# Kernel optimization log

Hardware: AMD Instinct MI355X
Metric: run time of the kernel (lower is better)

Reference implementation:

```python
import jax, jax.numpy as jnp
import numpy as np

N_NODES = 50000
N_EDGES = 800000
D = 128
BATCHSIZE = 64


def setup_inputs() -> dict:
    key = jax.random.key(0)
    k1, k2, k3, k4 = jax.random.split(key, 4)
    x = jax.random.normal(k1, (N_NODES, D), dtype=jnp.float32)
    eps = jnp.zeros((1,), dtype=jnp.float32)
    W_pred = jax.random.normal(k2, (D, D), dtype=jnp.float32) * (1.0 / np.sqrt(D))
    b_pred = jnp.zeros((D,), dtype=jnp.float32)
    edge_index = jax.random.randint(k3, (2, N_EDGES), 0, N_NODES, dtype=jnp.int64)
    batch = jnp.sort(jax.random.randint(k4, (N_NODES,), 0, BATCHSIZE, dtype=jnp.int64))
    return {"x": x, "eps": eps, "W_pred": W_pred, "b_pred": b_pred,
            "edge_index": edge_index, "batch": batch}


def reference(x, eps, W_pred, b_pred, edge_index, batch):
    src, dst = edge_index[0], edge_index[1]
    # spmm: sum of neighbor features for each destination node [N, D]
    agg = jax.ops.segment_sum(x[src], dst, num_segments=N_NODES)
    # eps-weighted self update (apply_func=None, norm=None)
    out = (1.0 + eps) * x + agg
    out = jax.nn.relu(out)  # activation='relu'
    # linear_prediction then per-graph scatter-add pooling
    pooled = out @ W_pred + b_pred  # [N, pooled_features]
    pooled2 = jax.ops.segment_sum(pooled, batch, num_segments=BATCHSIZE)  # [B, pooled]
    return out, pooled2
```

## Files before the change

kernel.cpp:

```cpp
#include <hip/hip_runtime.h>
#include <hip/hip_bf16.h>

#define N_NODES 50000
#define N_EDGES 800000
#define D 128
#define BATCHSIZE 64

#define CHUNK_BITS 7
#define CHUNK 128
#define NBUCKETS 391
#define NBUCKETS_PAD 392
#define CAP 2400

#define FB_TILE 4096
#define NTILES ((N_EDGES + FB_TILE - 1) / FB_TILE)
#define SLICES 4
#define SLICE_B 98
#define FB_THREADS 256
#define FB_GRID (NTILES * SLICES)

#define GB_THREADS 512
#define HCAP 1536

__device__ inline unsigned short f2bf(float f) {
    union { float f; unsigned u; } c; c.f = f;
    unsigned u = c.u;
    return (unsigned short)((u + 0x7fffu + ((u >> 16) & 1u)) >> 16);
}

__device__ inline float4 bf4_to_f4(uint2 u) {
    union { unsigned u; float f; } a, b, c, d;
    a.u = u.x << 16; b.u = u.x & 0xffff0000u;
    c.u = u.y << 16; d.u = u.y & 0xffff0000u;
    float4 r; r.x = a.f; r.y = b.f; r.z = c.f; r.w = d.f;
    return r;
}

__device__ inline int lower_bound_dev(const int* __restrict__ a, int n, int key) {
    int lo = 0, hi = n;
    while (lo < hi) {
        int mid = (lo + hi) >> 1;
        if (a[mid] < key) lo = mid + 1; else hi = mid;
    }
    return lo;
}

__global__ __launch_bounds__(FB_THREADS) void bin_convert_kernel(
    const float* __restrict__ x,
    unsigned short* __restrict__ xb,
    const int* __restrict__ edge_index,
    int* __restrict__ gcur,
    int* __restrict__ bucket,
    float* __restrict__ pooled2)
{
    __shared__ int hist[SLICE_B];
    __shared__ int gbase[SLICE_B];

    int t = threadIdx.x;
    int blk = blockIdx.x;

    for (int i = blk * FB_THREADS + t; i < BATCHSIZE * D; i += FB_GRID * FB_THREADS)
        pooled2[i] = 0.0f;

    if (xb != nullptr) {
        const int TOT4 = N_NODES * D / 4;
        for (int i = blk * FB_THREADS + t; i < TOT4; i += FB_GRID * FB_THREADS) {
            float4 v = *(const float4*)(x + (size_t)i * 4);
            uint2 pk;
            pk.x = (unsigned)f2bf(v.x) | ((unsigned)f2bf(v.y) << 16);
            pk.y = (unsigned)f2bf(v.z) | ((unsigned)f2bf(v.w) << 16);
            *(uint2*)(xb + (size_t)i * 4) = pk;
        }
    }

    int tile = blk >> 2;
    int sl   = blk & 3;
    int blo  = sl * SLICE_B;
    int bhi  = blo + SLICE_B; if (bhi > NBUCKETS) bhi = NBUCKETS;
    int nb   = bhi - blo;

    for (int i = t; i < SLICE_B; i += FB_THREADS) hist[i] = 0;
    __syncthreads();

    int base = tile * FB_TILE;
    int lim = N_EDGES - base; if (lim > FB_TILE) lim = FB_TILE;

    int bkt[16];
    int pack[16];
#pragma unroll
    for (int j = 0; j < 4; ++j) {
        int rel = j * FB_THREADS + t;
        int e4 = rel * 4;
#pragma unroll
        for (int k = 0; k < 4; ++k) bkt[j * 4 + k] = -1;
        if (e4 < lim) {
            int4 s4 = *(const int4*)(edge_index + base + e4);
            int4 d4 = *(const int4*)(edge_index + N_EDGES + base + e4);
            int ss[4] = { s4.x, s4.y, s4.z, s4.w };
            int dd[4] = { d4.x, d4.y, d4.z, d4.w };
#pragma unroll
            for (int k = 0; k < 4; ++k) {
                int b = (dd[k] >> CHUNK_BITS) - blo;
                if ((unsigned)b < (unsigned)nb) {
                    bkt[j * 4 + k] = b;
                    pack[j * 4 + k] = (ss[k] << CHUNK_BITS) | (dd[k] & (CHUNK - 1));
                    atomicAdd(&hist[b], 1);
                }
            }
        }
    }
    __syncthreads();

    for (int i = t; i < nb; i += FB_THREADS) {
        int c = hist[i];
        gbase[i] = c ? atomicAdd(&gcur[blo + i], c) : 0;
        hist[i] = 0;
    }
    __syncthreads();

#pragma unroll
    for (int k = 0; k < 16; ++k) {
        int b = bkt[k];
        if (b >= 0) {
            int pos = gbase[b] + atomicAdd(&hist[b], 1);
            if (pos < CAP) bucket[(size_t)(blo + b) * CAP + pos] = pack[k];
        }
    }
}

template<bool BF16>
__global__ __launch_bounds__(GB_THREADS) void gather_kernel(
    const float* __restrict__ x,
    const unsigned short* __restrict__ xb,
    const float* __restrict__ eps,
    const int* __restrict__ batch,
    const int* __restrict__ gcur,
    const int* __restrict__ bucket,
    const float* __restrict__ W,
    const float* __restrict__ b_pred,
    float* __restrict__ out,
    float* __restrict__ pooled2)
{
    __shared__ int   ebuf[CAP];
    __shared__ int   sorted[HCAP];
    __shared__ int   hist[64];
    __shared__ int   offs[65];
    __shared__ int   cursor[64];
    __shared__ float pool[8 * D];
    __shared__ int   pcount[8];

    int blk = blockIdx.x;
    int c = blk >> 1;
    int h = blk & 1;
    int t = threadIdx.x;
    int lane = t & 31;
    int g = t >> 5;

    if (t < 64) hist[t] = 0;
    if (t < 8) pcount[t] = 0;
    for (int i = t; i < 8 * D; i += GB_THREADS) pool[i] = 0.0f;
    int cnt = gcur[c];
    if (cnt > CAP) cnt = CAP;
    __syncthreads();

    for (int i = t; i < cnt; i += GB_THREADS) {
        int p = bucket[(size_t)c * CAP + i];
        ebuf[i] = p;
        int dl = p & (CHUNK - 1);
        if ((dl >> 6) == h) atomicAdd(&hist[dl & 63], 1);
    }
    __syncthreads();

    if (t < 64) {
        int v = hist[t];
        int incl = v;
#pragma unroll
        for (int o = 1; o < 64; o <<= 1) {
            int y = __shfl_up(incl, o, 64);
            if (t >= o) incl += y;
        }
        offs[t] = incl - v;
        cursor[t] = incl - v;
        if (t == 63) offs[64] = incl;
    }
    __syncthreads();

    for (int i = t; i < cnt; i += GB_THREADS) {
        int p = ebuf[i];
        int dl = p & (CHUNK - 1);
        if ((dl >> 6) == h) {
            int pos = atomicAdd(&cursor[dl & 63], 1);
            if (pos < HCAP) sorted[pos] = p >> CHUNK_BITS;
        }
    }
    __syncthreads();

    int node0 = (c << CHUNK_BITS) + (h << 6);
    int base_b = batch[node0 < N_NODES ? node0 : N_NODES - 1];
    float scale = 1.0f + eps[0];
    int dv_cur = -1;
    float4 ps = make_float4(0.f, 0.f, 0.f, 0.f);

#pragma unroll
    for (int k = 0; k < 4; ++k) {
        int d = 4 * g + k;
        int node = node0 + d;
        if (node >= N_NODES) break;
        int start = offs[d], end = offs[d + 1];
        if (end > HCAP) end = HCAP;
        float4 acc = make_float4(0.f, 0.f, 0.f, 0.f);
        int i = start;
        if (BF16) {
            for (; i + 4 <= end; i += 4) {
                int s0 = sorted[i], s1 = sorted[i + 1];
                int s2 = sorted[i + 2], s3 = sorted[i + 3];
                uint2 u0 = *(const uint2*)(xb + (size_t)s0 * D + lane * 4);
                uint2 u1 = *(const uint2*)(xb + (size_t)s1 * D + lane * 4);
                uint2 u2 = *(const uint2*)(xb + (size_t)s2 * D + lane * 4);
                uint2 u3 = *(const uint2*)(xb + (size_t)s3 * D + lane * 4);
                float4 v0 = bf4_to_f4(u0), v1 = bf4_to_f4(u1);
                float4 v2 = bf4_to_f4(u2), v3 = bf4_to_f4(u3);
                acc.x += (v0.x + v1.x) + (v2.x + v3.x);
                acc.y += (v0.y + v1.y) + (v2.y + v3.y);
                acc.z += (v0.z + v1.z) + (v2.z + v3.z);
                acc.w += (v0.w + v1.w) + (v2.w + v3.w);
            }
            for (; i < end; ++i) {
                uint2 u0 = *(const uint2*)(xb + (size_t)sorted[i] * D + lane * 4);
                float4 v0 = bf4_to_f4(u0);
                acc.x += v0.x; acc.y += v0.y; acc.z += v0.z; acc.w += v0.w;
            }
        } else {
            for (; i + 4 <= end; i += 4) {
                int s0 = sorted[i], s1 = sorted[i + 1];
                int s2 = sorted[i + 2], s3 = sorted[i + 3];
                const float4 v0 = *(const float4*)(x + (size_t)s0 * D + lane * 4);
                const float4 v1 = *(const float4*)(x + (size_t)s1 * D + lane * 4);
                const float4 v2 = *(const float4*)(x + (size_t)s2 * D + lane * 4);
                const float4 v3 = *(const float4*)(x + (size_t)s3 * D + lane * 4);
                acc.x += (v0.x + v1.x) + (v2.x + v3.x);
                acc.y += (v0.y + v1.y) + (v2.y + v3.y);
                acc.z += (v0.z + v1.z) + (v2.z + v3.z);
                acc.w += (v0.w + v1.w) + (v2.w + v3.w);
            }
            for (; i < end; ++i) {
                const float4 v0 = *(const float4*)(x + (size_t)sorted[i] * D + lane * 4);
                acc.x += v0.x; acc.y += v0.y; acc.z += v0.z; acc.w += v0.w;
            }
        }
        const float4 xv = *(const float4*)(x + (size_t)node * D + lane * 4);
        float4 o;
        o.x = fmaxf(fmaf(scale, xv.x, acc.x), 0.0f);
        o.y = fmaxf(fmaf(scale, xv.y, acc.y), 0.0f);
        o.z = fmaxf(fmaf(scale, xv.z, acc.z), 0.0f);
        o.w = fmaxf(fmaf(scale, xv.w, acc.w), 0.0f);
        *(float4*)(out + (size_t)node * D + lane * 4) = o;

        int dv = batch[node] - base_b;
        if (dv < 8) {
            if (dv != dv_cur) {
                if (dv_cur >= 0) {
                    float* pp = &pool[dv_cur * D + lane * 4];
                    atomicAdd(pp + 0, ps.x); atomicAdd(pp + 1, ps.y);
                    atomicAdd(pp + 2, ps.z); atomicAdd(pp + 3, ps.w);
                }
                ps = make_float4(0.f, 0.f, 0.f, 0.f);
                dv_cur = dv;
            }
            ps.x += o.x; ps.y += o.y; ps.z += o.z; ps.w += o.w;
            if (lane == 0) atomicAdd(&pcount[dv], 1);
        }
    }
    if (dv_cur >= 0) {
        float* pp = &pool[dv_cur * D + lane * 4];
        atomicAdd(pp + 0, ps.x); atomicAdd(pp + 1, ps.y);
        atomicAdd(pp + 2, ps.z); atomicAdd(pp + 3, ps.w);
    }
    __syncthreads();

    int lastnode = node0 + 63;
    if (lastnode >= N_NODES) lastnode = N_NODES - 1;
    int used = batch[lastnode] - base_b + 1;
    if (used > 8) used = 8;
    if (t < D) {
        for (int dv = 0; dv < used; ++dv) {
            float acc = (float)pcount[dv] * b_pred[t];
            const float* prow = &pool[dv * D];
#pragma unroll 8
            for (int k = 0; k < D; ++k) {
                acc = fmaf(prow[k], W[(size_t)k * D + t], acc);
            }
            atomicAdd(&pooled2[(size_t)(base_b + dv) * D + t], acc);
        }
    }
}


__global__ void edge_scatter_kernel(const float* __restrict__ x,
                                    const int* __restrict__ edge_index,
                                    float* __restrict__ agg) {
    int tid = blockIdx.x * blockDim.x + threadIdx.x;
    int lane = tid & 31;
    int e = tid >> 5;
    if (e >= N_EDGES) return;
    int src = edge_index[e];
    int dst = edge_index[N_EDGES + e];
    const float4 v = *(const float4*)(x + (size_t)src * D + lane * 4);
    float* dp = agg + (size_t)dst * D + lane * 4;
    atomicAdd(dp + 0, v.x);
    atomicAdd(dp + 1, v.y);
    atomicAdd(dp + 2, v.z);
    atomicAdd(dp + 3, v.w);
}

__global__ void finalize_kernel(const float* __restrict__ x,
                                const float* __restrict__ eps,
                                const int* __restrict__ batch,
                                float* __restrict__ out,
                                float* __restrict__ Sf,
                                float* __restrict__ counts) {
    int tid = blockIdx.x * blockDim.x + threadIdx.x;
    int lane = tid & 31;
    int node = tid >> 5;
    if (node >= N_NODES) return;
    float scale = 1.0f + eps[0];
    const float4 xv = *(const float4*)(x + (size_t)node * D + lane * 4);
    float4 av = *(float4*)(out + (size_t)node * D + lane * 4);
    float4 o;
    o.x = fmaxf(fmaf(scale, xv.x, av.x), 0.0f);
    o.y = fmaxf(fmaf(scale, xv.y, av.y), 0.0f);
    o.z = fmaxf(fmaf(scale, xv.z, av.z), 0.0f);
    o.w = fmaxf(fmaf(scale, xv.w, av.w), 0.0f);
    *(float4*)(out + (size_t)node * D + lane * 4) = o;
    int b = batch[node];
    float* sp = Sf + (size_t)b * D + lane * 4;
    atomicAdd(sp + 0, o.x);
    atomicAdd(sp + 1, o.y);
    atomicAdd(sp + 2, o.z);
    atomicAdd(sp + 3, o.w);
    if (lane == 0) atomicAdd(counts + b, 1.0f);
}

__global__ void pool_gemm_fallback_kernel(const float* __restrict__ Sf,
                                          const float* __restrict__ counts,
                                          const float* __restrict__ W,
                                          const float* __restrict__ b_pred,
                                          float* __restrict__ pooled2) {
    int b = blockIdx.x;
    int j = threadIdx.x;
    float acc = counts[b] * b_pred[j];
    const float* srow = Sf + (size_t)b * D;
#pragma unroll 8
    for (int k = 0; k < D; ++k) {
        acc = fmaf(srow[k], W[(size_t)k * D + j], acc);
    }
    pooled2[(size_t)b * D + j] = acc;
}

extern "C" void kernel_launch(void* const* d_in, const int* in_sizes, int n_in,
                              void* d_out, int out_size, void* d_ws, size_t ws_size,
                              hipStream_t stream) {
    const float* x      = (const float*)d_in[0];
    const float* eps    = (const float*)d_in[1];
    const float* W_pred = (const float*)d_in[2];
    const float* b_pred = (const float*)d_in[3];
    const int*   eidx   = (const int*)d_in[4];
    const int*   batch  = (const int*)d_in[5];

    float* out     = (float*)d_out;
    float* pooled2 = (float*)d_out + (size_t)N_NODES * D;

    const size_t base_ints = (size_t)NBUCKETS_PAD + (size_t)NBUCKETS * CAP;
    const size_t need_mid  = base_ints * 4;
    const size_t need_full = (base_ints + (size_t)N_NODES * D / 2) * 4;

    if (ws_size >= need_mid) {
        int* gcur   = (int*)d_ws;
        int* bucket = (int*)d_ws + NBUCKETS_PAD;
        bool full = (ws_size >= need_full);
        unsigned short* xb = full ? (unsigned short*)((int*)d_ws + base_ints) : nullptr;

        hipMemsetAsync(gcur, 0, (size_t)NBUCKETS_PAD * 4, stream);

        bin_convert_kernel<<<FB_GRID, FB_THREADS, 0, stream>>>(
            x, xb, eidx, gcur, bucket, pooled2);
        if (full) {
            gather_kernel<true><<<NBUCKETS * 2, GB_THREADS, 0, stream>>>(
                x, xb, eps, batch, gcur, bucket, W_pred, b_pred, out, pooled2);
        } else {
            gather_kernel<false><<<NBUCKETS * 2, GB_THREADS, 0, stream>>>(
                x, (const unsigned short*)nullptr, eps, batch, gcur, bucket,
                W_pred, b_pred, out, pooled2);
        }
    } else {
        float* Sf      = (float*)d_ws;
        float* countsf = (float*)d_ws + BATCHSIZE * D;
        hipMemsetAsync(out, 0, (size_t)N_NODES * D * sizeof(float), stream);
        hipMemsetAsync(d_ws, 0, (BATCHSIZE * D + BATCHSIZE) * sizeof(float), stream);
        {
            long long total = (long long)N_EDGES * 32;
            int blocks = (int)((total + 255) / 256);
            edge_scatter_kernel<<<blocks, 256, 0, stream>>>(x, eidx, out);
        }
        {
            long long total = (long long)N_NODES * 32;
            int blocks = (int)((total + 255) / 256);
            finalize_kernel<<<blocks, 256, 0, stream>>>(x, eps, batch, out, Sf, countsf);
        }
        pool_gemm_fallback_kernel<<<BATCHSIZE, D, 0, stream>>>(Sf, countsf, W_pred, b_pred, pooled2);
    }
}
```

Baseline: 157.3 us.

## Process each 128-node bucket in one 1024-thread block instead of two halves

The gather kernel now launches one 1024-thread block per bucket instead of two 512-thread blocks that each handled half of the bucket's nodes. This removes the duplicated load and filtering of the bucket's edge list and the per-half histogram, and each bucket's edges are now sorted once over all 128 nodes. In exchange the grid is halved to 391 blocks, and larger blocks with more shared memory can lower occupancy and load balance on a GPU with many compute units. The pooled projection runs once per bucket rather than once per half.

```diff
diff --git a/kernel.cpp b/kernel.cpp
--- a/kernel.cpp
+++ b/kernel.cpp
@@ -19,9 +19,6 @@
 #define FB_THREADS 256
 #define FB_GRID (NTILES * SLICES)
 
-#define GB_THREADS 512
-#define HCAP 1536
-
 __device__ inline unsigned short f2bf(float f) {
     union { float f; unsigned u; } c; c.f = f;
     unsigned u = c.u;
@@ -34,15 +31,6 @@
     c.u = u.y << 16; d.u = u.y & 0xffff0000u;
     float4 r; r.x = a.f; r.y = b.f; r.z = c.f; r.w = d.f;
     return r;
-}
-
-__device__ inline int lower_bound_dev(const int* __restrict__ a, int n, int key) {
-    int lo = 0, hi = n;
-    while (lo < hi) {
-        int mid = (lo + hi) >> 1;
-        if (a[mid] < key) lo = mid + 1; else hi = mid;
-    }
-    return lo;
 }
 
 __global__ __launch_bounds__(FB_THREADS) void bin_convert_kernel(
@@ -129,7 +117,7 @@
 }
 
 template<bool BF16>
-__global__ __launch_bounds__(GB_THREADS) void gather_kernel(
+__global__ __launch_bounds__(1024) void gather_kernel(
     const float* __restrict__ x,
     const unsigned short* __restrict__ xb,
     const float* __restrict__ eps,
@@ -142,61 +130,57 @@
     float* __restrict__ pooled2)
 {
     __shared__ int   ebuf[CAP];
-    __shared__ int   sorted[HCAP];
-    __shared__ int   hist[64];
-    __shared__ int   offs[65];
-    __shared__ int   cursor[64];
+    __shared__ int   sorted[CAP];
+    __shared__ int   hist[CHUNK];
+    __shared__ int   offs[CHUNK + 1];
+    __shared__ int   cursor[CHUNK];
     __shared__ float pool[8 * D];
     __shared__ int   pcount[8];
 
-    int blk = blockIdx.x;
-    int c = blk >> 1;
-    int h = blk & 1;
+    int c = blockIdx.x;
     int t = threadIdx.x;
     int lane = t & 31;
     int g = t >> 5;
 
-    if (t < 64) hist[t] = 0;
+    if (t < CHUNK) hist[t] = 0;
     if (t < 8) pcount[t] = 0;
-    for (int i = t; i < 8 * D; i += GB_THREADS) pool[i] = 0.0f;
+    for (int i = t; i < 8 * D; i += 1024) pool[i] = 0.0f;
     int cnt = gcur[c];
     if (cnt > CAP) cnt = CAP;
     __syncthreads();
 
-    for (int i = t; i < cnt; i += GB_THREADS) {
+    for (int i = t; i < cnt; i += 1024) {
         int p = bucket[(size_t)c * CAP + i];
         ebuf[i] = p;
-        int dl = p & (CHUNK - 1);
-        if ((dl >> 6) == h) atomicAdd(&hist[dl & 63], 1);
+        atomicAdd(&hist[p & (CHUNK - 1)], 1);
     }
     __syncthreads();
 
     if (t < 64) {
-        int v = hist[t];
-        int incl = v;
+        int h0 = hist[2 * t], h1 = hist[2 * t + 1];
+        int tot = h0 + h1;
+        int incl = tot;
 #pragma unroll
         for (int o = 1; o < 64; o <<= 1) {
             int y = __shfl_up(incl, o, 64);
             if (t >= o) incl += y;
         }
-        offs[t] = incl - v;
-        cursor[t] = incl - v;
-        if (t == 63) offs[64] = incl;
-    }
-    __syncthreads();
-
-    for (int i = t; i < cnt; i += GB_THREADS) {
+        int excl = incl - tot;
+        offs[2 * t] = excl;          cursor[2 * t] = excl;
+        offs[2 * t + 1] = excl + h0; cursor[2 * t + 1] = excl + h0;
+        if (t == 63) offs[CHUNK] = incl;
+    }
+    __syncthreads();
+
+    for (int i = t; i < cnt; i += 1024) {
         int p = ebuf[i];
-        int dl = p & (CHUNK - 1);
-        if ((dl >> 6) == h) {
-            int pos = atomicAdd(&cursor[dl & 63], 1);
-            if (pos < HCAP) sorted[pos] = p >> CHUNK_BITS;
-        }
-    }
-    __syncthreads();
-
-    int node0 = (c << CHUNK_BITS) + (h << 6);
-    int base_b = batch[node0 < N_NODES ? node0 : N_NODES - 1];
+        int pos = atomicAdd(&cursor[p & (CHUNK - 1)], 1);
+        sorted[pos] = p >> CHUNK_BITS;
+    }
+    __syncthreads();
+
+    int node0 = c << CHUNK_BITS;
+    int base_b = batch[node0];
     float scale = 1.0f + eps[0];
     int dv_cur = -1;
     float4 ps = make_float4(0.f, 0.f, 0.f, 0.f);
@@ -207,7 +191,6 @@
         int node = node0 + d;
         if (node >= N_NODES) break;
         int start = offs[d], end = offs[d + 1];
-        if (end > HCAP) end = HCAP;
         float4 acc = make_float4(0.f, 0.f, 0.f, 0.f);
         int i = start;
         if (BF16) {
@@ -278,7 +261,7 @@
     }
     __syncthreads();
 
-    int lastnode = node0 + 63;
+    int lastnode = node0 + CHUNK - 1;
     if (lastnode >= N_NODES) lastnode = N_NODES - 1;
     int used = batch[lastnode] - base_b + 1;
     if (used > 8) used = 8;
@@ -385,10 +368,10 @@
         bin_convert_kernel<<<FB_GRID, FB_THREADS, 0, stream>>>(
             x, xb, eidx, gcur, bucket, pooled2);
         if (full) {
-            gather_kernel<true><<<NBUCKETS * 2, GB_THREADS, 0, stream>>>(
+            gather_kernel<true><<<NBUCKETS, 1024, 0, stream>>>(
                 x, xb, eps, batch, gcur, bucket, W_pred, b_pred, out, pooled2);
         } else {
-            gather_kernel<false><<<NBUCKETS * 2, GB_THREADS, 0, stream>>>(
+            gather_kernel<false><<<NBUCKETS, 1024, 0, stream>>>(
                 x, (const unsigned short*)nullptr, eps, batch, gcur, bucket,
                 W_pred, b_pred, out, pooled2);
         }
```

Measured after the change: 155.8 us. About the same (-0.9%).
